# Performance work log

Measured on AMD Instinct MI355X. Metric: run time of the kernel, lower is better.

## Reference

```python
import jax, jax.numpy as jnp
import numpy as np

BN_EPS = 1e-5


def setup_inputs() -> dict:
    key = jax.random.key(0)
    ks = jax.random.split(key, 6)
    N, C, T, V, S = 64, 64, 300, 25, 3
    x = jax.random.normal(ks[0], (N, C, T, V), dtype=jnp.float32)
    A = jax.random.uniform(ks[1], (S, V, V), dtype=jnp.float32)
    PA1 = jnp.ones((S, V, V), dtype=jnp.float32)
    PA2 = jax.random.normal(ks[2], (S, V, V), dtype=jnp.float32) * 1e-3
    Wc = jax.random.normal(ks[3], (S, C, C), dtype=jnp.float32) * np.sqrt(2.0 / (C * S))
    bc = jnp.zeros((S, C), dtype=jnp.float32)
    gamma = jnp.ones((C,), dtype=jnp.float32)
    beta = jnp.zeros((C,), dtype=jnp.float32)
    rmean = jnp.zeros((C,), dtype=jnp.float32)
    rvar = jnp.ones((C,), dtype=jnp.float32)
    return {"x": x, "A": A, "PA1": PA1, "PA2": PA2, "Wc": Wc, "bc": bc,
            "gamma": gamma, "beta": beta, "rmean": rmean, "rvar": rvar}


def reference(x, A, PA1, PA2, Wc, bc, gamma, beta, rmean, rvar):
    # x: (N, C, T, V); A/PA1/PA2: (S, V, V); Wc: (S, out_c, in_c); bc: (S, out_c)
    Ae = A * PA1 + PA2  # adaptive adjacency, (S, V, V)
    S = Ae.shape[0]
    y = None
    for i in range(S):  # small fixed loop over graph subsets
        # graph aggregation over joints: (N,C,T,V) @ (V,V) -> (N,C,T,V)
        xa = jnp.einsum('nctv,vw->nctw', x, Ae[i])
        # 1x1 conv over channels + bias
        z = jnp.einsum('nctw,oc->notw', xa, Wc[i]) + bc[i][None, :, None, None]
        y = z if y is None else y + z
    # BatchNorm2d (inference form with running stats)
    scale = gamma / jnp.sqrt(rvar + BN_EPS)
    y = y * scale[None, :, None, None] + (beta - rmean * scale)[None, :, None, None]
    # residual: in_channels == out_channels -> down is identity
    y = y + x
    return jax.nn.relu(y)
```

## Files before the change

### kernel.cpp

```cpp
#include <hip/hip_runtime.h>

typedef _Float16 half_t;
typedef __attribute__((ext_vector_type(8))) _Float16 half8;
typedef __attribute__((ext_vector_type(4))) _Float16 half4;
typedef __attribute__((ext_vector_type(4))) float float4_t;

#define BN_EPS 1e-5f

constexpr int Nn = 64, Cc = 64, Tt = 300, Vv = 25, Ss = 3;
constexpr int TB   = 8;
constexpr int TWN  = TB * Vv;
constexpr int NT   = 13;
constexpr int XL_T = 32;
constexpr int XL_C = TB * XL_T + 8;
constexpr int XA_S = 72;
constexpr int XA_R = NT * 16;
constexpr int AE_S = 40;

__global__ __launch_bounds__(256, 2)
void gcn_fused(const float* __restrict__ x,   const float* __restrict__ A,
               const float* __restrict__ PA1, const float* __restrict__ PA2,
               const float* __restrict__ Wc,  const float* __restrict__ bc,
               const float* __restrict__ gamma, const float* __restrict__ beta,
               const float* __restrict__ rmean, const float* __restrict__ rvar,
               float* __restrict__ out)
{
    __shared__ __align__(16) half_t Xl[Cc * XL_C];
    __shared__ __align__(16) half_t xaL[XA_R * XA_S];
    __shared__ __align__(16) half_t AeT[Ss * 32 * AE_S];
    __shared__ float bnsc[Cc], bnsh[Cc];

    const int tid  = threadIdx.x;
    const int lane = tid & 63;
    const int wave = tid >> 6;
    const int col  = lane & 15;
    const int quad = lane >> 4;

    const int tb = blockIdx.x;
    const int n  = blockIdx.y;
    const int t0 = tb * TB;

    if (tid < Cc) {
        float sc   = gamma[tid] * rsqrtf(rvar[tid] + BN_EPS);
        float bsum = bc[tid] + bc[Cc + tid] + bc[2 * Cc + tid];
        bnsc[tid] = sc;
        bnsh[tid] = beta[tid] - rmean[tid] * sc + bsum * sc;
    }

    for (int e = tid; e < Ss * 32 * 32; e += 256) {
        int s = e >> 10, r = e & 1023, w = r >> 5, v = r & 31;
        float val = 0.f;
        if (v < Vv && w < Vv) {
            int ai = (s * Vv + v) * Vv + w;
            val = A[ai] * PA1[ai] + PA2[ai];
        }
        AeT[(s * 32 + w) * AE_S + v] = (half_t)val;
    }

    for (int e = tid; e < (XA_R - TWN) * XA_S; e += 256)
        xaL[TWN * XA_S + e] = (half_t)0.f;

    half8 wf[Ss][2];
    {
        int o = wave * 16 + col;
        #pragma unroll
        for (int s = 0; s < Ss; ++s)
            #pragma unroll
            for (int ks = 0; ks < 2; ++ks) {
                const float* p = Wc + (s * Cc + o) * Cc + ks * 32 + quad * 8;
                half8 h;
                #pragma unroll
                for (int j = 0; j < 8; ++j) h[j] = (half_t)p[j];
                wf[s][ks] = h;
            }
    }

    {
        const float* xb = x + (size_t)n * Cc * Tt * Vv + t0 * Vv;
        for (int slot = tid; slot < Cc * TB * 8; slot += 256) {
            int c = slot >> 6, rem = slot & 63, t = rem >> 3, k = rem & 7;
            int v0 = k * 4;
            half4 h;
            #pragma unroll
            for (int j = 0; j < 4; ++j) {
                int v = v0 + j;
                float f = (v < Vv && (t0 + t) < Tt) ? xb[c * Tt * Vv + t * Vv + v] : 0.f;
                h[j] = (half_t)f;
            }
            *(half4*)&Xl[c * XL_C + t * XL_T + v0] = h;
        }
    }
    __syncthreads();

    const float4_t zero4 = {0.f, 0.f, 0.f, 0.f};
    float4_t yacc[NT];
    #pragma unroll
    for (int i = 0; i < NT; ++i) yacc[i] = zero4;

    for (int s = 0; s < Ss; ++s) {
        half8 ab[2];
        #pragma unroll
        for (int wt = 0; wt < 2; ++wt)
            ab[wt] = *(const half8*)&AeT[(s * 32 + wt * 16 + col) * AE_S + quad * 8];

        #pragma unroll
        for (int ti = 0; ti < 2; ++ti) {
            int t = wave * 2 + ti;
            #pragma unroll
            for (int ct = 0; ct < 4; ++ct) {
                half8 af = *(const half8*)&Xl[(ct * 16 + col) * XL_C + t * XL_T + quad * 8];
                #pragma unroll
                for (int wt = 0; wt < 2; ++wt) {
                    float4_t r = __builtin_amdgcn_mfma_f32_16x16x32_f16(af, ab[wt], zero4, 0, 0, 0);
                    int w = wt * 16 + col;
                    if (w < Vv) {
                        half4 h;
                        #pragma unroll
                        for (int i = 0; i < 4; ++i) h[i] = (half_t)r[i];
                        *(half4*)&xaL[(t * Vv + w) * XA_S + ct * 16 + quad * 4] = h;
                    }
                }
            }
        }
        __syncthreads();

        #pragma unroll
        for (int nt = 0; nt < NT; ++nt) {
            int tw = nt * 16 + col;
            #pragma unroll
            for (int ks = 0; ks < 2; ++ks) {
                half8 bf = *(const half8*)&xaL[tw * XA_S + ks * 32 + quad * 8];
                yacc[nt] = __builtin_amdgcn_mfma_f32_16x16x32_f16(wf[s][ks], bf, yacc[nt], 0, 0, 0);
            }
        }
        __syncthreads();
    }

    const int limit = min(TWN, (Tt - t0) * Vv);
    float* ob = out + (size_t)n * Cc * Tt * Vv + t0 * Vv;
    #pragma unroll
    for (int nt = 0; nt < NT; ++nt) {
        int tw = nt * 16 + col;
        if (tw < limit) {
            int t = tw / Vv;
            int w = tw - t * Vv;
            #pragma unroll
            for (int i = 0; i < 4; ++i) {
                int o = wave * 16 + quad * 4 + i;
                float val = yacc[nt][i] * bnsc[o] + bnsh[o];
                val += (float)Xl[o * XL_C + t * XL_T + w];
                ob[o * Tt * Vv + tw] = fmaxf(val, 0.f);
            }
        }
    }
}

extern "C" void kernel_launch(void* const* d_in, const int* in_sizes, int n_in,
                              void* d_out, int out_size, void* d_ws, size_t ws_size,
                              hipStream_t stream) {
    const float* x     = (const float*)d_in[0];
    const float* A     = (const float*)d_in[1];
    const float* PA1   = (const float*)d_in[2];
    const float* PA2   = (const float*)d_in[3];
    const float* Wc    = (const float*)d_in[4];
    const float* bc    = (const float*)d_in[5];
    const float* gamma = (const float*)d_in[6];
    const float* beta  = (const float*)d_in[7];
    const float* rmean = (const float*)d_in[8];
    const float* rvar  = (const float*)d_in[9];
    float* out = (float*)d_out;

    dim3 grid((Tt + TB - 1) / TB, Nn);
    gcn_fused<<<grid, 256, 0, stream>>>(x, A, PA1, PA2, Wc, bc, gamma, beta, rmean, rvar, out);
}
```

Measured before the change: 354.6 us.

## Halve time tile, keep adjacency in registers, raise occupancy to four blocks

```diff
diff --git a/kernel.cpp b/kernel.cpp
--- a/kernel.cpp
+++ b/kernel.cpp
@@ -3,21 +3,21 @@
 typedef _Float16 half_t;
 typedef __attribute__((ext_vector_type(8))) _Float16 half8;
 typedef __attribute__((ext_vector_type(4))) _Float16 half4;
+typedef __attribute__((ext_vector_type(2))) _Float16 half2_t;
 typedef __attribute__((ext_vector_type(4))) float float4_t;
 
 #define BN_EPS 1e-5f
 
 constexpr int Nn = 64, Cc = 64, Tt = 300, Vv = 25, Ss = 3;
-constexpr int TB   = 8;
+constexpr int TB   = 4;
 constexpr int TWN  = TB * Vv;
-constexpr int NT   = 13;
+constexpr int NT   = 7;
 constexpr int XL_T = 32;
 constexpr int XL_C = TB * XL_T + 8;
 constexpr int XA_S = 72;
 constexpr int XA_R = NT * 16;
-constexpr int AE_S = 40;
 
-__global__ __launch_bounds__(256, 2)
+__global__ __launch_bounds__(256, 4)
 void gcn_fused(const float* __restrict__ x,   const float* __restrict__ A,
                const float* __restrict__ PA1, const float* __restrict__ PA2,
                const float* __restrict__ Wc,  const float* __restrict__ bc,
@@ -27,7 +27,6 @@
 {
     __shared__ __align__(16) half_t Xl[Cc * XL_C];
     __shared__ __align__(16) half_t xaL[XA_R * XA_S];
-    __shared__ __align__(16) half_t AeT[Ss * 32 * AE_S];
     __shared__ float bnsc[Cc], bnsh[Cc];
 
     const int tid  = threadIdx.x;
@@ -47,14 +46,18 @@
         bnsh[tid] = beta[tid] - rmean[tid] * sc + bsum * sc;
     }
 
-    for (int e = tid; e < Ss * 32 * 32; e += 256) {
-        int s = e >> 10, r = e & 1023, w = r >> 5, v = r & 31;
-        float val = 0.f;
-        if (v < Vv && w < Vv) {
-            int ai = (s * Vv + v) * Vv + w;
-            val = A[ai] * PA1[ai] + PA2[ai];
+    {
+        const float* xb = x + (size_t)n * Cc * Tt * Vv + t0 * Vv;
+        #pragma unroll
+        for (int i = 0; i < 16; ++i) {
+            int e = tid + i * 256;
+            int c = e >> 6, r = e & 63, t = r >> 4, v0 = (r & 15) * 2;
+            const float* p = xb + c * (Tt * Vv) + t * Vv + v0;
+            float f0 = (v0     < Vv) ? p[0] : 0.f;
+            float f1 = (v0 + 1 < Vv) ? p[1] : 0.f;
+            half2_t hh = { (half_t)f0, (half_t)f1 };
+            *(half2_t*)&Xl[c * XL_C + t * XL_T + v0] = hh;
         }
-        AeT[(s * 32 + w) * AE_S + v] = (half_t)val;
     }
 
     for (int e = tid; e < (XA_R - TWN) * XA_S; e += 256)
@@ -75,21 +78,26 @@
             }
     }
 
-    {
-        const float* xb = x + (size_t)n * Cc * Tt * Vv + t0 * Vv;
-        for (int slot = tid; slot < Cc * TB * 8; slot += 256) {
-            int c = slot >> 6, rem = slot & 63, t = rem >> 3, k = rem & 7;
-            int v0 = k * 4;
-            half4 h;
+    half8 ab[Ss][2];
+    #pragma unroll
+    for (int s = 0; s < Ss; ++s)
+        #pragma unroll
+        for (int wt = 0; wt < 2; ++wt) {
+            int w = wt * 16 + col;
+            half8 h;
             #pragma unroll
-            for (int j = 0; j < 4; ++j) {
-                int v = v0 + j;
-                float f = (v < Vv && (t0 + t) < Tt) ? xb[c * Tt * Vv + t * Vv + v] : 0.f;
-                h[j] = (half_t)f;
+            for (int j = 0; j < 8; ++j) {
+                int v = quad * 8 + j;
+                float val = 0.f;
+                if (v < Vv && w < Vv) {
+                    int ai = (s * Vv + v) * Vv + w;
+                    val = A[ai] * PA1[ai] + PA2[ai];
+                }
+                h[j] = (half_t)val;
             }
-            *(half4*)&Xl[c * XL_C + t * XL_T + v0] = h;
+            ab[s][wt] = h;
         }
-    }
+
     __syncthreads();
 
     const float4_t zero4 = {0.f, 0.f, 0.f, 0.f};
@@ -98,20 +106,14 @@
     for (int i = 0; i < NT; ++i) yacc[i] = zero4;
 
     for (int s = 0; s < Ss; ++s) {
-        half8 ab[2];
-        #pragma unroll
-        for (int wt = 0; wt < 2; ++wt)
-            ab[wt] = *(const half8*)&AeT[(s * 32 + wt * 16 + col) * AE_S + quad * 8];
-
-        #pragma unroll
-        for (int ti = 0; ti < 2; ++ti) {
-            int t = wave * 2 + ti;
+        {
+            const int t = wave;
             #pragma unroll
             for (int ct = 0; ct < 4; ++ct) {
                 half8 af = *(const half8*)&Xl[(ct * 16 + col) * XL_C + t * XL_T + quad * 8];
                 #pragma unroll
                 for (int wt = 0; wt < 2; ++wt) {
-                    float4_t r = __builtin_amdgcn_mfma_f32_16x16x32_f16(af, ab[wt], zero4, 0, 0, 0);
+                    float4_t r = __builtin_amdgcn_mfma_f32_16x16x32_f16(af, ab[s][wt], zero4, 0, 0, 0);
                     int w = wt * 16 + col;
                     if (w < Vv) {
                         half4 h;
@@ -133,15 +135,14 @@
                 yacc[nt] = __builtin_amdgcn_mfma_f32_16x16x32_f16(wf[s][ks], bf, yacc[nt], 0, 0, 0);
             }
         }
-        __syncthreads();
+        if (s < Ss - 1) __syncthreads();
     }
 
-    const int limit = min(TWN, (Tt - t0) * Vv);
     float* ob = out + (size_t)n * Cc * Tt * Vv + t0 * Vv;
     #pragma unroll
     for (int nt = 0; nt < NT; ++nt) {
         int tw = nt * 16 + col;
-        if (tw < limit) {
+        if (tw < TWN) {
             int t = tw / Vv;
             int w = tw - t * Vv;
             #pragma unroll
@@ -170,6 +171,6 @@
     const float* rvar  = (const float*)d_in[9];
     float* out = (float*)d_out;
 
-    dim3 grid((Tt + TB - 1) / TB, Nn);
+    dim3 grid(Tt / TB, Nn);
     gcn_fused<<<grid, 256, 0, stream>>>(x, A, PA1, PA2, Wc, bc, gamma, beta, rmean, rvar, out);
 }
```

Result: slower. 380.5 us (+7.3%).
